# Kernel optimization log

Measured on AMD Instinct MI355X. Metric: run time of the kernel, lower is better.

Reference implementation:

```python
import jax, jax.numpy as jnp
import numpy as np

N_NODES = 100000
N_EDGES = 800000
D = 64
N_ITERS = 3  # n_layers - 1


def setup_inputs() -> dict:
    key = jax.random.key(0)
    k1, k2, k3, k4 = jax.random.split(key, 4)
    x = jax.random.normal(k1, (N_NODES, D), dtype=jnp.float32)
    edge_index = jax.random.randint(k2, (2, N_EDGES), 0, N_NODES, dtype=jnp.int64)
    edge_weight = jax.random.uniform(k3, (N_EDGES,), dtype=jnp.float32)
    # Linear(64, 64) weight, scaled ~ kaiming so 3 stacked layers stay bounded
    W = jax.random.normal(k4, (D, D), dtype=jnp.float32) * (1.0 / np.sqrt(D))
    b = jnp.zeros((D,), dtype=jnp.float32)
    return {"x": x, "edge_index": edge_index, "edge_weight": edge_weight, "W": W, "b": b}


def reference(x, edge_index, edge_weight, W, b):
    # Faithful math of RPINetEncoder.forward: (n_layers-1) iterations of
    # LinearAggregation (weighted scatter-add message passing + shared Linear)
    # followed by ReLU. Dropout output is discarded in the original -> no-op.
    src = edge_index[0]
    dst = edge_index[1]
    n = x.shape[0]
    for _ in range(N_ITERS):
        msgs = edge_weight[:, None] * x[src]                      # [E, D] gather
        agg = jax.ops.segment_sum(msgs, dst, num_segments=n)      # [N, D] scatter-add
        x = jax.nn.relu(agg @ W.T + b)                            # shared linear + relu
    return x
```

## Files before the change

### kernel.cpp

```cpp
#include <hip/hip_runtime.h>
#include <hip/hip_bf16.h>

#define D 64
#define FP_SCALE 262144.0f
#define FP_INV   (1.0f / 262144.0f)
#define NPC 64
#define ASTR 65

__device__ __forceinline__ unsigned short f2bf(float f) {
    unsigned int u = __float_as_uint(f);
    u += 0x7fffu + ((u >> 16) & 1u);
    return (unsigned short)(u >> 16);
}

__global__ void hist_kernel(const int* __restrict__ dst, int* __restrict__ counts, int E) {
    int e = blockIdx.x * blockDim.x + threadIdx.x;
    if (e < E) atomicAdd(&counts[dst[e]], 1);
}

__global__ void part_kernel(const int* __restrict__ counts, int* __restrict__ partial, int N) {
    __shared__ int ws4[4];
    int t = threadIdx.x, lane = t & 63, w = t >> 6;
    int n = blockIdx.x * 256 + t;
    int c = (n < N) ? counts[n] : 0;
    #pragma unroll
    for (int off = 32; off > 0; off >>= 1) c += __shfl_down(c, off);
    if (lane == 0) ws4[w] = c;
    __syncthreads();
    if (t == 0) partial[blockIdx.x] = ws4[0] + ws4[1] + ws4[2] + ws4[3];
}

__global__ void scan_kernel(int* __restrict__ partial, int nb) {
    __shared__ int wsum[8];
    int t = threadIdx.x, lane = t & 63, w = t >> 6;
    int carry = 0;
    for (int base = 0; base < nb; base += 512) {
        int i = base + t;
        int v = (i < nb) ? partial[i] : 0;
        int incl = v;
        #pragma unroll
        for (int off = 1; off < 64; off <<= 1) {
            int x = __shfl_up(incl, off);
            if (lane >= off) incl += x;
        }
        if (lane == 63) wsum[w] = incl;
        __syncthreads();
        int wpre = 0;
        for (int j = 0; j < w; ++j) wpre += wsum[j];
        int tot = 0;
        for (int j = 0; j < 8; ++j) tot += wsum[j];
        if (i < nb) partial[i] = carry + wpre + incl - v;
        carry += tot;
        __syncthreads();
    }
}

__global__ void seg_kernel(const int* __restrict__ counts, const int* __restrict__ partial,
                           int* __restrict__ cursor, int* __restrict__ blockStart, int N) {
    __shared__ int ws4[4];
    int t = threadIdx.x, lane = t & 63, w = t >> 6;
    int n = blockIdx.x * 256 + t;
    int c = (n < N) ? counts[n] : 0;
    int incl = c;
    #pragma unroll
    for (int off = 1; off < 64; off <<= 1) {
        int x = __shfl_up(incl, off);
        if (lane >= off) incl += x;
    }
    if (lane == 63) ws4[w] = incl;
    __syncthreads();
    int wpre = 0;
    for (int j = 0; j < w; ++j) wpre += ws4[j];
    int st = partial[blockIdx.x] + wpre + incl - c;
    if (n < N) {
        cursor[n] = st;
        if ((n & (NPC - 1)) == 0) blockStart[n / NPC] = st;
    }
}

__global__ void fill_kernel(const int* __restrict__ src, const int* __restrict__ dst,
                            const float* __restrict__ ew, int* __restrict__ cursor,
                            unsigned long long* __restrict__ perm64, int E) {
    int e = blockIdx.x * blockDim.x + threadIdx.x;
    if (e < E) {
        int d = dst[e];
        int p = atomicAdd(&cursor[d], 1);
        unsigned lo = ((unsigned)src[e] << 6) | (unsigned)(d & (NPC - 1));
        perm64[p] = ((unsigned long long)__float_as_uint(ew[e] * FP_SCALE) << 32) | lo;
    }
}

__global__ void cvt_kernel(const float* __restrict__ in, unsigned short* __restrict__ out, int n4) {
    int i = blockIdx.x * blockDim.x + threadIdx.x;
    if (i >= n4) return;
    float4 v = reinterpret_cast<const float4*>(in)[i];
    ushort4 o;
    o.x = f2bf(v.x); o.y = f2bf(v.y); o.z = f2bf(v.z); o.w = f2bf(v.w);
    reinterpret_cast<ushort4*>(out)[i] = o;
}

template<bool OUT_BF>
__global__ void agg_fused_kernel(const unsigned short* __restrict__ xb,
                                 const unsigned long long* __restrict__ perm64,
                                 const int* __restrict__ blockStart,
                                 const float* __restrict__ W,
                                 const float* __restrict__ bias,
                                 void* __restrict__ xout,
                                 int N, int E) {
    __shared__ int acc[NPC * ASTR];
    __shared__ float Wt[D][D];
    __shared__ float bsh[D];
    int t = threadIdx.x;
    int bid = blockIdx.x;
    int nodeBase = bid * NPC;
    int nodeEnd = min(nodeBase + NPC, N);
    int es = blockStart[bid];
    int ee = (bid + 1 < (int)gridDim.x) ? blockStart[bid + 1] : E;

    for (int i = t; i < NPC * ASTR / 4; i += 256)
        reinterpret_cast<int4*>(acc)[i] = make_int4(0, 0, 0, 0);
    for (int i = t; i < D * D; i += 256) {
        int j = i >> 6, d = i & 63;
        Wt[d][j] = W[i] * FP_INV;
    }
    if (t < D) bsh[t] = bias[t];
    __syncthreads();

    int g = t >> 4;
    int i16 = t & 15;
    int gl = g & 3;
    int w4 = g >> 2;

#define EDGE_ATOMIC(pk)                                                         \
    {                                                                           \
        unsigned lo_ = (unsigned)(pk);                                          \
        float w_ = __uint_as_float((unsigned)((pk) >> 32));                     \
        int slot_ = (int)(lo_ & (NPC - 1));                                     \
        int s_ = (int)(lo_ >> 6);                                               \
        uint2 u_ = *reinterpret_cast<const uint2*>(&xb[(size_t)s_ * D + (i16 << 2)]); \
        int base_ = slot_ * ASTR + i16;                                         \
        atomicAdd(&acc[base_ +  0], (int)(w_ * __uint_as_float(u_.x << 16)));   \
        atomicAdd(&acc[base_ + 16], (int)(w_ * __uint_as_float(u_.x & 0xffff0000u))); \
        atomicAdd(&acc[base_ + 32], (int)(w_ * __uint_as_float(u_.y << 16)));   \
        atomicAdd(&acc[base_ + 48], (int)(w_ * __uint_as_float(u_.y & 0xffff0000u))); \
    }

    int myOff = es + gl * 16 + w4 * 4;
    int cnt = ee - es;
    int kmax = cnt >> 6;
    for (int k = 0; k < kmax; ++k) {
        int e0 = myOff + (k << 6);
        unsigned long long pk0 = perm64[e0 + 0];
        unsigned long long pk1 = perm64[e0 + 1];
        unsigned long long pk2 = perm64[e0 + 2];
        unsigned long long pk3 = perm64[e0 + 3];
        EDGE_ATOMIC(pk0); EDGE_ATOMIC(pk1); EDGE_ATOMIC(pk2); EDGE_ATOMIC(pk3);
    }
    for (int e = es + (kmax << 6) + g; e < ee; e += 16) {
        unsigned long long pk = perm64[e];
        EDGE_ATOMIC(pk);
    }
#undef EDGE_ATOMIC
    __syncthreads();

    int wave = t >> 6, lane = t & 63;
    int sBase = wave * 16;
    float o[16];
    #pragma unroll
    for (int i = 0; i < 16; ++i) o[i] = 0.f;
    for (int q = 0; q < 16; ++q) {
        float w0 = Wt[4 * q + 0][lane];
        float w1 = Wt[4 * q + 1][lane];
        float w2 = Wt[4 * q + 2][lane];
        float w3 = Wt[4 * q + 3][lane];
        #pragma unroll
        for (int i = 0; i < 16; ++i) {
            int base = (sBase + i) * ASTR + q;
            float a0 = (float)acc[base +  0];
            float a1 = (float)acc[base + 16];
            float a2 = (float)acc[base + 32];
            float a3 = (float)acc[base + 48];
            o[i] = fmaf(a0, w0, fmaf(a1, w1, fmaf(a2, w2, fmaf(a3, w3, o[i]))));
        }
    }
    #pragma unroll
    for (int i = 0; i < 16; ++i) {
        int node = nodeBase + sBase + i;
        if (node < nodeEnd) {
            float v = fmaxf(bsh[lane] + o[i], 0.0f);
            size_t off = (size_t)node * D + lane;
            if (OUT_BF) ((unsigned short*)xout)[off] = f2bf(v);
            else        ((float*)xout)[off] = v;
        }
    }
}

__global__ void rpi_scatter_kernel(const float* __restrict__ x,
                                   const int* __restrict__ src,
                                   const int* __restrict__ dst,
                                   const float* __restrict__ ew,
                                   int* __restrict__ agg, int E) {
    int tid = blockIdx.x * blockDim.x + threadIdx.x;
    int e = tid >> 4;
    if (e >= E) return;
    int c = (tid & 15) << 2;
    int s = src[e], d = dst[e];
    float w = ew[e] * FP_SCALE;
    float4 v = *reinterpret_cast<const float4*>(&x[(size_t)s * D + c]);
    int* o = &agg[(size_t)d * D + c];
    atomicAdd(o + 0, (int)(w * v.x));
    atomicAdd(o + 1, (int)(w * v.y));
    atomicAdd(o + 2, (int)(w * v.z));
    atomicAdd(o + 3, (int)(w * v.w));
}

__global__ void rpi_linear_relu_kernel(const int* __restrict__ agg,
                                       const float* __restrict__ W,
                                       const float* __restrict__ b,
                                       float* __restrict__ out, int N) {
    __shared__ float Ws[D][D + 1];
    __shared__ float bs[D];
    int t = threadIdx.x;
    for (int i = t; i < D * D; i += 256) Ws[i >> 6][i & 63] = W[i];
    if (t < D) bs[t] = b[t];
    __syncthreads();
    int wave = t >> 6, lane = t & 63;
    int nwaves = gridDim.x * 4;
    for (int n = blockIdx.x * 4 + wave; n < N; n += nwaves) {
        const int* arow = &agg[(size_t)n * D];
        float acc = bs[lane];
        #pragma unroll
        for (int d = 0; d < D; ++d) acc = fmaf((float)arow[d] * FP_INV, Ws[lane][d], acc);
        out[(size_t)n * D + lane] = fmaxf(acc, 0.0f);
    }
}

extern "C" void kernel_launch(void* const* d_in, const int* in_sizes, int n_in,
                              void* d_out, int out_size, void* d_ws, size_t ws_size,
                              hipStream_t stream) {
    const float* x0 = (const float*)d_in[0];
    const int*   ei = (const int*)d_in[1];
    const float* ew = (const float*)d_in[2];
    const float* W  = (const float*)d_in[3];
    const float* b  = (const float*)d_in[4];
    float* out = (float*)d_out;

    int N = in_sizes[0] / D;
    int E = in_sizes[2];
    const int* src = ei;
    const int* dst = ei + E;

    int nb   = (N + 255) / 256;
    int nblk = (N + NPC - 1) / NPC;
    size_t xeb = (size_t)N * D * sizeof(unsigned short);
    size_t off = 0;
    size_t o_xb1  = off; off += xeb;
    size_t o_xb2  = off; off += xeb;
    size_t o_p64  = off; off += (size_t)E * sizeof(unsigned long long);
    size_t o_cnt  = off; off += (size_t)N * sizeof(int);
    size_t o_part = off; off += ((size_t)nb + 16) * sizeof(int);
    size_t o_bs   = off; off += ((size_t)nblk + 2) * sizeof(int);
    size_t need = off;

    if (ws_size >= need) {
        unsigned short* xb1 = (unsigned short*)((char*)d_ws + o_xb1);
        unsigned short* xb2 = (unsigned short*)((char*)d_ws + o_xb2);
        unsigned long long* perm64 = (unsigned long long*)((char*)d_ws + o_p64);
        int* cnt_cur    = (int*)((char*)d_ws + o_cnt);
        int* partial    = (int*)((char*)d_ws + o_part);
        int* blockStart = (int*)((char*)d_ws + o_bs);

        int eb = (E + 255) / 256;
        int n4 = N * D / 4;

        hipMemsetAsync(cnt_cur, 0, (size_t)N * sizeof(int), stream);
        hist_kernel<<<eb, 256, 0, stream>>>(dst, cnt_cur, E);
        part_kernel<<<nb, 256, 0, stream>>>(cnt_cur, partial, N);
        scan_kernel<<<1, 512, 0, stream>>>(partial, nb);
        seg_kernel <<<nb, 256, 0, stream>>>(cnt_cur, partial, cnt_cur, blockStart, N);
        fill_kernel<<<eb, 256, 0, stream>>>(src, dst, ew, cnt_cur, perm64, E);
        cvt_kernel <<<(n4 + 255) / 256, 256, 0, stream>>>(x0, xb1, n4);

        agg_fused_kernel<true> <<<nblk, 256, 0, stream>>>(xb1, perm64, blockStart, W, b, xb2, N, E);
        agg_fused_kernel<true> <<<nblk, 256, 0, stream>>>(xb2, perm64, blockStart, W, b, xb1, N, E);
        agg_fused_kernel<false><<<nblk, 256, 0, stream>>>(xb1, perm64, blockStart, W, b, out, N, E);
    } else {
        int* agg = (int*)d_ws;
        const float* xcur = x0;
        int sb = (E * 16 + 255) / 256;
        for (int it = 0; it < 3; ++it) {
            hipMemsetAsync(agg, 0, (size_t)N * D * sizeof(int), stream);
            rpi_scatter_kernel<<<sb, 256, 0, stream>>>(xcur, src, dst, ew, agg, E);
            rpi_linear_relu_kernel<<<2048, 256, 0, stream>>>(agg, W, b, out, N);
            xcur = out;
        }
    }
}
```

Baseline: 313.7 us.

## Bucket edges per 32-node chunk, drop per-node scan and bf16 pre-conversion

Edges are now grouped by 32-node chunk rather than sorted per node. The histogram, scan and fill work at chunk granularity, which replaces the part/scan/seg chain with a single scan kernel and shrinks the atomic counter array. The first layer reads fp32 x directly, so the separate bf16 conversion kernel is gone, at the cost of wider gathers in that layer. Halving NPC doubles the block count and rebalances each block's edges across its four groups, with smaller blocks giving less reuse of the W load per block.

```diff
diff --git a/kernel.cpp b/kernel.cpp
--- a/kernel.cpp
+++ b/kernel.cpp
@@ -4,7 +4,8 @@
 #define D 64
 #define FP_SCALE 262144.0f
 #define FP_INV   (1.0f / 262144.0f)
-#define NPC 64
+#define NPC 32
+#define LOG_NPC 5
 #define ASTR 65
 
 __device__ __forceinline__ unsigned short f2bf(float f) {
@@ -13,30 +14,19 @@
     return (unsigned short)(u >> 16);
 }
 
-__global__ void hist_kernel(const int* __restrict__ dst, int* __restrict__ counts, int E) {
+__global__ void hist_kernel(const int* __restrict__ dst, int* __restrict__ chunkCnt, int E) {
     int e = blockIdx.x * blockDim.x + threadIdx.x;
-    if (e < E) atomicAdd(&counts[dst[e]], 1);
-}
-
-__global__ void part_kernel(const int* __restrict__ counts, int* __restrict__ partial, int N) {
-    __shared__ int ws4[4];
-    int t = threadIdx.x, lane = t & 63, w = t >> 6;
-    int n = blockIdx.x * 256 + t;
-    int c = (n < N) ? counts[n] : 0;
-    #pragma unroll
-    for (int off = 32; off > 0; off >>= 1) c += __shfl_down(c, off);
-    if (lane == 0) ws4[w] = c;
-    __syncthreads();
-    if (t == 0) partial[blockIdx.x] = ws4[0] + ws4[1] + ws4[2] + ws4[3];
-}
-
-__global__ void scan_kernel(int* __restrict__ partial, int nb) {
+    if (e < E) atomicAdd(&chunkCnt[dst[e] >> LOG_NPC], 1);
+}
+
+__global__ void scan_kernel(const int* __restrict__ chunkCnt, int* __restrict__ blockStart,
+                            int* __restrict__ cursor, int nblk) {
     __shared__ int wsum[8];
     int t = threadIdx.x, lane = t & 63, w = t >> 6;
     int carry = 0;
-    for (int base = 0; base < nb; base += 512) {
+    for (int base = 0; base < nblk; base += 512) {
         int i = base + t;
-        int v = (i < nb) ? partial[i] : 0;
+        int v = (i < nblk) ? chunkCnt[i] : 0;
         int incl = v;
         #pragma unroll
         for (int off = 1; off < 64; off <<= 1) {
@@ -49,32 +39,13 @@
         for (int j = 0; j < w; ++j) wpre += wsum[j];
         int tot = 0;
         for (int j = 0; j < 8; ++j) tot += wsum[j];
-        if (i < nb) partial[i] = carry + wpre + incl - v;
+        if (i < nblk) {
+            int st = carry + wpre + incl - v;
+            blockStart[i] = st;
+            cursor[i] = st;
+        }
         carry += tot;
         __syncthreads();
-    }
-}
-
-__global__ void seg_kernel(const int* __restrict__ counts, const int* __restrict__ partial,
-                           int* __restrict__ cursor, int* __restrict__ blockStart, int N) {
-    __shared__ int ws4[4];
-    int t = threadIdx.x, lane = t & 63, w = t >> 6;
-    int n = blockIdx.x * 256 + t;
-    int c = (n < N) ? counts[n] : 0;
-    int incl = c;
-    #pragma unroll
-    for (int off = 1; off < 64; off <<= 1) {
-        int x = __shfl_up(incl, off);
-        if (lane >= off) incl += x;
-    }
-    if (lane == 63) ws4[w] = incl;
-    __syncthreads();
-    int wpre = 0;
-    for (int j = 0; j < w; ++j) wpre += ws4[j];
-    int st = partial[blockIdx.x] + wpre + incl - c;
-    if (n < N) {
-        cursor[n] = st;
-        if ((n & (NPC - 1)) == 0) blockStart[n / NPC] = st;
     }
 }
 
@@ -84,23 +55,14 @@
     int e = blockIdx.x * blockDim.x + threadIdx.x;
     if (e < E) {
         int d = dst[e];
-        int p = atomicAdd(&cursor[d], 1);
-        unsigned lo = ((unsigned)src[e] << 6) | (unsigned)(d & (NPC - 1));
+        int p = atomicAdd(&cursor[d >> LOG_NPC], 1);
+        unsigned lo = ((unsigned)src[e] << LOG_NPC) | (unsigned)(d & (NPC - 1));
         perm64[p] = ((unsigned long long)__float_as_uint(ew[e] * FP_SCALE) << 32) | lo;
     }
 }
 
-__global__ void cvt_kernel(const float* __restrict__ in, unsigned short* __restrict__ out, int n4) {
-    int i = blockIdx.x * blockDim.x + threadIdx.x;
-    if (i >= n4) return;
-    float4 v = reinterpret_cast<const float4*>(in)[i];
-    ushort4 o;
-    o.x = f2bf(v.x); o.y = f2bf(v.y); o.z = f2bf(v.z); o.w = f2bf(v.w);
-    reinterpret_cast<ushort4*>(out)[i] = o;
-}
-
-template<bool OUT_BF>
-__global__ void agg_fused_kernel(const unsigned short* __restrict__ xb,
+template<bool IN_F32, bool OUT_BF>
+__global__ void agg_fused_kernel(const void* __restrict__ xin,
                                  const unsigned long long* __restrict__ perm64,
                                  const int* __restrict__ blockStart,
                                  const float* __restrict__ W,
@@ -119,6 +81,8 @@
 
     for (int i = t; i < NPC * ASTR / 4; i += 256)
         reinterpret_cast<int4*>(acc)[i] = make_int4(0, 0, 0, 0);
+    if (t < NPC * ASTR - (NPC * ASTR / 4) * 4)
+        acc[(NPC * ASTR / 4) * 4 + t] = 0;
     for (int i = t; i < D * D; i += 256) {
         int j = i >> 6, d = i & 63;
         Wt[d][j] = W[i] * FP_INV;
@@ -136,45 +100,61 @@
         unsigned lo_ = (unsigned)(pk);                                          \
         float w_ = __uint_as_float((unsigned)((pk) >> 32));                     \
         int slot_ = (int)(lo_ & (NPC - 1));                                     \
-        int s_ = (int)(lo_ >> 6);                                               \
-        uint2 u_ = *reinterpret_cast<const uint2*>(&xb[(size_t)s_ * D + (i16 << 2)]); \
+        int s_ = (int)(lo_ >> LOG_NPC);                                         \
+        float v0_, v1_, v2_, v3_;                                               \
+        if (IN_F32) {                                                           \
+            float4 u_ = *reinterpret_cast<const float4*>(                       \
+                (const float*)xin + (size_t)s_ * D + (i16 << 2));               \
+            v0_ = u_.x; v1_ = u_.y; v2_ = u_.z; v3_ = u_.w;                     \
+        } else {                                                                \
+            uint2 u_ = *reinterpret_cast<const uint2*>(                         \
+                (const unsigned short*)xin + (size_t)s_ * D + (i16 << 2));      \
+            v0_ = __uint_as_float(u_.x << 16);                                  \
+            v1_ = __uint_as_float(u_.x & 0xffff0000u);                          \
+            v2_ = __uint_as_float(u_.y << 16);                                  \
+            v3_ = __uint_as_float(u_.y & 0xffff0000u);                          \
+        }                                                                       \
         int base_ = slot_ * ASTR + i16;                                         \
-        atomicAdd(&acc[base_ +  0], (int)(w_ * __uint_as_float(u_.x << 16)));   \
-        atomicAdd(&acc[base_ + 16], (int)(w_ * __uint_as_float(u_.x & 0xffff0000u))); \
-        atomicAdd(&acc[base_ + 32], (int)(w_ * __uint_as_float(u_.y << 16)));   \
-        atomicAdd(&acc[base_ + 48], (int)(w_ * __uint_as_float(u_.y & 0xffff0000u))); \
-    }
-
-    int myOff = es + gl * 16 + w4 * 4;
+        atomicAdd(&acc[base_ +  0], (int)(w_ * v0_));                           \
+        atomicAdd(&acc[base_ + 16], (int)(w_ * v1_));                           \
+        atomicAdd(&acc[base_ + 32], (int)(w_ * v2_));                           \
+        atomicAdd(&acc[base_ + 48], (int)(w_ * v3_));                           \
+    }
+
     int cnt = ee - es;
-    int kmax = cnt >> 6;
-    for (int k = 0; k < kmax; ++k) {
-        int e0 = myOff + (k << 6);
-        unsigned long long pk0 = perm64[e0 + 0];
-        unsigned long long pk1 = perm64[e0 + 1];
-        unsigned long long pk2 = perm64[e0 + 2];
-        unsigned long long pk3 = perm64[e0 + 3];
-        EDGE_ATOMIC(pk0); EDGE_ATOMIC(pk1); EDGE_ATOMIC(pk2); EDGE_ATOMIC(pk3);
-    }
-    for (int e = es + (kmax << 6) + g; e < ee; e += 16) {
-        unsigned long long pk = perm64[e];
-        EDGE_ATOMIC(pk);
+    int qlen = (cnt + 3) >> 2;
+    int qs = es + gl * qlen;
+    int qe = min(qs + qlen, ee);
+    for (int e = qs + w4 * 4; e < qe; e += 16) {
+        int m = min(4, qe - e);
+        if (m == 4) {
+            unsigned long long pk0 = perm64[e + 0];
+            unsigned long long pk1 = perm64[e + 1];
+            unsigned long long pk2 = perm64[e + 2];
+            unsigned long long pk3 = perm64[e + 3];
+            EDGE_ATOMIC(pk0); EDGE_ATOMIC(pk1); EDGE_ATOMIC(pk2); EDGE_ATOMIC(pk3);
+        } else {
+            for (int r = 0; r < m; ++r) {
+                unsigned long long pk = perm64[e + r];
+                EDGE_ATOMIC(pk);
+            }
+        }
     }
 #undef EDGE_ATOMIC
     __syncthreads();
 
     int wave = t >> 6, lane = t & 63;
-    int sBase = wave * 16;
-    float o[16];
+    int sBase = wave * (NPC / 4);
+    float o[NPC / 4];
     #pragma unroll
-    for (int i = 0; i < 16; ++i) o[i] = 0.f;
+    for (int i = 0; i < NPC / 4; ++i) o[i] = 0.f;
     for (int q = 0; q < 16; ++q) {
         float w0 = Wt[4 * q + 0][lane];
         float w1 = Wt[4 * q + 1][lane];
         float w2 = Wt[4 * q + 2][lane];
         float w3 = Wt[4 * q + 3][lane];
         #pragma unroll
-        for (int i = 0; i < 16; ++i) {
+        for (int i = 0; i < NPC / 4; ++i) {
             int base = (sBase + i) * ASTR + q;
             float a0 = (float)acc[base +  0];
             float a1 = (float)acc[base + 16];
@@ -184,7 +164,7 @@
         }
     }
     #pragma unroll
-    for (int i = 0; i < 16; ++i) {
+    for (int i = 0; i < NPC / 4; ++i) {
         int node = nodeBase + sBase + i;
         if (node < nodeEnd) {
             float v = fmaxf(bsh[lane] + o[i], 0.0f);
@@ -250,40 +230,35 @@
     const int* src = ei;
     const int* dst = ei + E;
 
-    int nb   = (N + 255) / 256;
     int nblk = (N + NPC - 1) / NPC;
     size_t xeb = (size_t)N * D * sizeof(unsigned short);
     size_t off = 0;
-    size_t o_xb1  = off; off += xeb;
-    size_t o_xb2  = off; off += xeb;
-    size_t o_p64  = off; off += (size_t)E * sizeof(unsigned long long);
-    size_t o_cnt  = off; off += (size_t)N * sizeof(int);
-    size_t o_part = off; off += ((size_t)nb + 16) * sizeof(int);
-    size_t o_bs   = off; off += ((size_t)nblk + 2) * sizeof(int);
+    size_t o_xb1 = off; off += xeb;
+    size_t o_xb2 = off; off += xeb;
+    size_t o_p64 = off; off += (size_t)E * sizeof(unsigned long long);
+    size_t o_cnt = off; off += (size_t)nblk * sizeof(int);
+    size_t o_bs  = off; off += ((size_t)nblk + 2) * sizeof(int);
+    size_t o_cur = off; off += ((size_t)nblk + 2) * sizeof(int);
     size_t need = off;
 
     if (ws_size >= need) {
         unsigned short* xb1 = (unsigned short*)((char*)d_ws + o_xb1);
         unsigned short* xb2 = (unsigned short*)((char*)d_ws + o_xb2);
         unsigned long long* perm64 = (unsigned long long*)((char*)d_ws + o_p64);
-        int* cnt_cur    = (int*)((char*)d_ws + o_cnt);
-        int* partial    = (int*)((char*)d_ws + o_part);
+        int* chunkCnt   = (int*)((char*)d_ws + o_cnt);
         int* blockStart = (int*)((char*)d_ws + o_bs);
+        int* cursor     = (int*)((char*)d_ws + o_cur);
 
         int eb = (E + 255) / 256;
-        int n4 = N * D / 4;
-
-        hipMemsetAsync(cnt_cur, 0, (size_t)N * sizeof(int), stream);
-        hist_kernel<<<eb, 256, 0, stream>>>(dst, cnt_cur, E);
-        part_kernel<<<nb, 256, 0, stream>>>(cnt_cur, partial, N);
-        scan_kernel<<<1, 512, 0, stream>>>(partial, nb);
-        seg_kernel <<<nb, 256, 0, stream>>>(cnt_cur, partial, cnt_cur, blockStart, N);
-        fill_kernel<<<eb, 256, 0, stream>>>(src, dst, ew, cnt_cur, perm64, E);
-        cvt_kernel <<<(n4 + 255) / 256, 256, 0, stream>>>(x0, xb1, n4);
-
-        agg_fused_kernel<true> <<<nblk, 256, 0, stream>>>(xb1, perm64, blockStart, W, b, xb2, N, E);
-        agg_fused_kernel<true> <<<nblk, 256, 0, stream>>>(xb2, perm64, blockStart, W, b, xb1, N, E);
-        agg_fused_kernel<false><<<nblk, 256, 0, stream>>>(xb1, perm64, blockStart, W, b, out, N, E);
+
+        hipMemsetAsync(chunkCnt, 0, (size_t)nblk * sizeof(int), stream);
+        hist_kernel<<<eb, 256, 0, stream>>>(dst, chunkCnt, E);
+        scan_kernel<<<1, 512, 0, stream>>>(chunkCnt, blockStart, cursor, nblk);
+        fill_kernel<<<eb, 256, 0, stream>>>(src, dst, ew, cursor, perm64, E);
+
+        agg_fused_kernel<true,  true> <<<nblk, 256, 0, stream>>>(x0,  perm64, blockStart, W, b, xb2, N, E);
+        agg_fused_kernel<false, true> <<<nblk, 256, 0, stream>>>(xb2, perm64, blockStart, W, b, xb1, N, E);
+        agg_fused_kernel<false, false><<<nblk, 256, 0, stream>>>(xb1, perm64, blockStart, W, b, out, N, E);
     } else {
         int* agg = (int*)d_ws;
         const float* xcur = x0;
```

New measurement: 358.8 us. +14.4%, slower.

## Fuse fp32 input read into first aggregation, store W as bf16, unroll 8

Applied to the files above, without the earlier changes.

Drops the separate fp32-to-bf16 conversion kernel: the first aggregation layer now gathers fp32 rows directly, and later layers keep their bf16 inputs. The shared-memory copy of the transposed weight matrix is stored as bf16 instead of fp32, which halves that LDS footprint but lowers the precision of the linear layer. The main edge loop now loads eight packed edges per iteration instead of four to put more gathers in flight. The fp32 gather in layer one reads twice the bytes per edge of the bf16 path, which may offset the saved launch and conversion pass.

```diff
diff --git a/kernel.cpp b/kernel.cpp
--- a/kernel.cpp
+++ b/kernel.cpp
@@ -90,17 +90,8 @@
     }
 }
 
-__global__ void cvt_kernel(const float* __restrict__ in, unsigned short* __restrict__ out, int n4) {
-    int i = blockIdx.x * blockDim.x + threadIdx.x;
-    if (i >= n4) return;
-    float4 v = reinterpret_cast<const float4*>(in)[i];
-    ushort4 o;
-    o.x = f2bf(v.x); o.y = f2bf(v.y); o.z = f2bf(v.z); o.w = f2bf(v.w);
-    reinterpret_cast<ushort4*>(out)[i] = o;
-}
-
-template<bool OUT_BF>
-__global__ void agg_fused_kernel(const unsigned short* __restrict__ xb,
+template<bool IN_F32, bool OUT_BF>
+__global__ void agg_fused_kernel(const void* __restrict__ xin,
                                  const unsigned long long* __restrict__ perm64,
                                  const int* __restrict__ blockStart,
                                  const float* __restrict__ W,
@@ -108,7 +99,7 @@
                                  void* __restrict__ xout,
                                  int N, int E) {
     __shared__ int acc[NPC * ASTR];
-    __shared__ float Wt[D][D];
+    __shared__ unsigned short Wtb[D][D];
     __shared__ float bsh[D];
     int t = threadIdx.x;
     int bid = blockIdx.x;
@@ -121,7 +112,7 @@
         reinterpret_cast<int4*>(acc)[i] = make_int4(0, 0, 0, 0);
     for (int i = t; i < D * D; i += 256) {
         int j = i >> 6, d = i & 63;
-        Wt[d][j] = W[i] * FP_INV;
+        Wtb[d][j] = f2bf(W[i] * FP_INV);
     }
     if (t < D) bsh[t] = bias[t];
     __syncthreads();
@@ -137,26 +128,43 @@
         float w_ = __uint_as_float((unsigned)((pk) >> 32));                     \
         int slot_ = (int)(lo_ & (NPC - 1));                                     \
         int s_ = (int)(lo_ >> 6);                                               \
-        uint2 u_ = *reinterpret_cast<const uint2*>(&xb[(size_t)s_ * D + (i16 << 2)]); \
+        float v0_, v1_, v2_, v3_;                                               \
+        if (IN_F32) {                                                           \
+            float4 u_ = *reinterpret_cast<const float4*>(                       \
+                (const float*)xin + (size_t)s_ * D + (i16 << 2));               \
+            v0_ = u_.x; v1_ = u_.y; v2_ = u_.z; v3_ = u_.w;                     \
+        } else {                                                                \
+            uint2 u_ = *reinterpret_cast<const uint2*>(                         \
+                (const unsigned short*)xin + (size_t)s_ * D + (i16 << 2));      \
+            v0_ = __uint_as_float(u_.x << 16);                                  \
+            v1_ = __uint_as_float(u_.x & 0xffff0000u);                          \
+            v2_ = __uint_as_float(u_.y << 16);                                  \
+            v3_ = __uint_as_float(u_.y & 0xffff0000u);                          \
+        }                                                                       \
         int base_ = slot_ * ASTR + i16;                                         \
-        atomicAdd(&acc[base_ +  0], (int)(w_ * __uint_as_float(u_.x << 16)));   \
-        atomicAdd(&acc[base_ + 16], (int)(w_ * __uint_as_float(u_.x & 0xffff0000u))); \
-        atomicAdd(&acc[base_ + 32], (int)(w_ * __uint_as_float(u_.y << 16)));   \
-        atomicAdd(&acc[base_ + 48], (int)(w_ * __uint_as_float(u_.y & 0xffff0000u))); \
-    }
-
-    int myOff = es + gl * 16 + w4 * 4;
+        atomicAdd(&acc[base_ +  0], (int)(w_ * v0_));                           \
+        atomicAdd(&acc[base_ + 16], (int)(w_ * v1_));                           \
+        atomicAdd(&acc[base_ + 32], (int)(w_ * v2_));                           \
+        atomicAdd(&acc[base_ + 48], (int)(w_ * v3_));                           \
+    }
+
+    int myOff = es + gl * 32 + w4 * 8;
     int cnt = ee - es;
-    int kmax = cnt >> 6;
+    int kmax = cnt >> 7;
     for (int k = 0; k < kmax; ++k) {
-        int e0 = myOff + (k << 6);
+        int e0 = myOff + (k << 7);
         unsigned long long pk0 = perm64[e0 + 0];
         unsigned long long pk1 = perm64[e0 + 1];
         unsigned long long pk2 = perm64[e0 + 2];
         unsigned long long pk3 = perm64[e0 + 3];
+        unsigned long long pk4 = perm64[e0 + 4];
+        unsigned long long pk5 = perm64[e0 + 5];
+        unsigned long long pk6 = perm64[e0 + 6];
+        unsigned long long pk7 = perm64[e0 + 7];
         EDGE_ATOMIC(pk0); EDGE_ATOMIC(pk1); EDGE_ATOMIC(pk2); EDGE_ATOMIC(pk3);
-    }
-    for (int e = es + (kmax << 6) + g; e < ee; e += 16) {
+        EDGE_ATOMIC(pk4); EDGE_ATOMIC(pk5); EDGE_ATOMIC(pk6); EDGE_ATOMIC(pk7);
+    }
+    for (int e = es + (kmax << 7) + g; e < ee; e += 16) {
         unsigned long long pk = perm64[e];
         EDGE_ATOMIC(pk);
     }
@@ -169,10 +177,10 @@
     #pragma unroll
     for (int i = 0; i < 16; ++i) o[i] = 0.f;
     for (int q = 0; q < 16; ++q) {
-        float w0 = Wt[4 * q + 0][lane];
-        float w1 = Wt[4 * q + 1][lane];
-        float w2 = Wt[4 * q + 2][lane];
-        float w3 = Wt[4 * q + 3][lane];
+        float w0 = __uint_as_float((unsigned)Wtb[4 * q + 0][lane] << 16);
+        float w1 = __uint_as_float((unsigned)Wtb[4 * q + 1][lane] << 16);
+        float w2 = __uint_as_float((unsigned)Wtb[4 * q + 2][lane] << 16);
+        float w3 = __uint_as_float((unsigned)Wtb[4 * q + 3][lane] << 16);
         #pragma unroll
         for (int i = 0; i < 16; ++i) {
             int base = (sBase + i) * ASTR + q;
@@ -271,7 +279,6 @@
         int* blockStart = (int*)((char*)d_ws + o_bs);
 
         int eb = (E + 255) / 256;
-        int n4 = N * D / 4;
 
         hipMemsetAsync(cnt_cur, 0, (size_t)N * sizeof(int), stream);
         hist_kernel<<<eb, 256, 0, stream>>>(dst, cnt_cur, E);
@@ -279,11 +286,10 @@
         scan_kernel<<<1, 512, 0, stream>>>(partial, nb);
         seg_kernel <<<nb, 256, 0, stream>>>(cnt_cur, partial, cnt_cur, blockStart, N);
         fill_kernel<<<eb, 256, 0, stream>>>(src, dst, ew, cnt_cur, perm64, E);
-        cvt_kernel <<<(n4 + 255) / 256, 256, 0, stream>>>(x0, xb1, n4);
-
-        agg_fused_kernel<true> <<<nblk, 256, 0, stream>>>(xb1, perm64, blockStart, W, b, xb2, N, E);
-        agg_fused_kernel<true> <<<nblk, 256, 0, stream>>>(xb2, perm64, blockStart, W, b, xb1, N, E);
-        agg_fused_kernel<false><<<nblk, 256, 0, stream>>>(xb1, perm64, blockStart, W, b, out, N, E);
+
+        agg_fused_kernel<true,  true> <<<nblk, 256, 0, stream>>>(x0,  perm64, blockStart, W, b, xb2, N, E);
+        agg_fused_kernel<false, true> <<<nblk, 256, 0, stream>>>(xb2, perm64, blockStart, W, b, xb1, N, E);
+        agg_fused_kernel<false, false><<<nblk, 256, 0, stream>>>(xb1, perm64, blockStart, W, b, out, N, E);
     } else {
         int* agg = (int*)d_ws;
         const float* xcur = x0;
```

Measured after the change: 302.2 us, median of 2. 3.7% less time.
